# Kernel tuning notes

Hardware: AMD Instinct MI355X
Metric: run time of the kernel (lower is better)

## Reference

```python
import jax, jax.numpy as jnp
import numpy as np

B = 4096        # batch
KD = 64         # koopman_dim
NC = 24         # complex eigenvalue pairs
NR = 16         # real eigenvalues (KD = 2*NC + NR)
DT = 0.01       # delta_t
LC = 2 * NC     # complex net latent/out dim
LR = NR         # real net latent/out dim


def setup_inputs() -> dict:
    key = jax.random.key(0)
    ks = jax.random.split(key, 9)
    def w(k, o, i):
        return jax.random.normal(k, (o, i), dtype=jnp.float32) / np.sqrt(i)
    return {
        "x": jax.random.normal(ks[0], (B, 1, KD), dtype=jnp.float32),
        "Wc1": w(ks[1], LC, KD), "bc1": jnp.zeros((LC,), jnp.float32),
        "Wc2": w(ks[2], LC, LC), "bc2": jnp.zeros((LC,), jnp.float32),
        "Wr1": w(ks[3], LR, KD), "br1": jnp.zeros((LR,), jnp.float32),
        "Wr2": w(ks[4], LR, LR), "br2": jnp.zeros((LR,), jnp.float32),
        "T": 256,
    }


def reference(x, Wc1, bc1, Wc2, bc2, Wr1, br1, Wr2, br2, T):
    # Sequential Koopman rollout. Instead of materializing the [B,KD,KD]
    # block-diagonal K each step, apply the 2x2 rotation*decay blocks and the
    # real decay directly (identical math, no dense matmul).
    dt = jnp.float32(DT)

    def step(y, _):
        # complex parametrization MLP: [B,KD] -> [B,2*NC]
        co = jnp.tanh(y @ Wc1.T + bc1) @ Wc2.T + bc2
        co = co.reshape(-1, NC, 2)
        mu, omega = co[..., 0], co[..., 1]          # [B,NC] each
        scale = jnp.exp(dt * mu)
        c = jnp.cos(dt * omega) * scale             # cos*exp
        s = jnp.sin(dt * omega) * scale             # sin*exp
        yc = y[:, :2 * NC].reshape(-1, NC, 2)       # paired complex coords
        new_c = jnp.stack(
            [c * yc[..., 0] - s * yc[..., 1],
             s * yc[..., 0] + c * yc[..., 1]], axis=-1
        ).reshape(-1, 2 * NC)
        # real parametrization MLP: [B,KD] -> [B,NR]
        re = jnp.tanh(y @ Wr1.T + br1) @ Wr2.T + br2
        new_r = jnp.exp(dt * re) * y[:, 2 * NC:]
        y_new = jnp.concatenate([new_c, new_r], axis=-1)
        return y_new, y_new

    y0 = x[:, 0, :]
    _, Ys = jax.lax.scan(step, y0, None, length=T)  # [T,B,KD]
    return jnp.swapaxes(Ys, 0, 1)                   # [B,T,KD]
```

## Files before the change

kernel.cpp:

```cpp
#include <hip/hip_runtime.h>

#define NB    4096
#define TSTEP 256
#define EPB   8
#define DTC   0.01f

typedef _Float16 h8 __attribute__((ext_vector_type(8)));
typedef _Float16 h4 __attribute__((ext_vector_type(4)));
typedef float    f4 __attribute__((ext_vector_type(4)));

__device__ __forceinline__ float fast_tanh(float a) {
    float t = fminf(a * 2.885390082f, 126.0f);
    float E = __builtin_amdgcn_exp2f(t);
    return (E - 1.0f) * __builtin_amdgcn_rcpf(E + 1.0f);
}
__device__ __forceinline__ float texp(float m) {
    return fmaf(m, fmaf(m, fmaf(m, 1.0f/6.0f, 0.5f), 1.0f), 1.0f);
}

__device__ __forceinline__ void lds_barrier() {
    asm volatile("s_waitcnt lgkmcnt(0)" ::: "memory");
    __builtin_amdgcn_s_barrier();
    asm volatile("" ::: "memory");
}

#define U16B  2304

__global__ void __launch_bounds__(256)
koopman_kernel(const float* __restrict__ x,
               const float* __restrict__ Wc1, const float* __restrict__ bc1,
               const float* __restrict__ Wc2, const float* __restrict__ bc2,
               const float* __restrict__ Wr1, const float* __restrict__ br1,
               const float* __restrict__ Wr2, const float* __restrict__ br2,
               float* __restrict__ out)
{
    const int tid  = threadIdx.x;
    const int lane = tid & 63;
    const int w    = tid >> 6;
    const int blk  = blockIdx.x;

    __shared__ __align__(16) unsigned char L[U16B * 2];

    const int e  = lane & 15;
    const int es = e & (EPB - 1);
    const int g  = lane >> 4;

    const int fa = 16*w + e;
    h8 a1lo, a1hi, a2lo, a2hi;
    {
        const float* r1 = (fa < 48) ? (Wc1 + fa*64) : (Wr1 + (fa-48)*64);
        #pragma unroll
        for (int i = 0; i < 8; ++i) {
            a1lo[i] = (_Float16)r1[8*g + i];
            a1hi[i] = (_Float16)r1[32 + 8*g + i];
        }
        #pragma unroll
        for (int i = 0; i < 8; ++i) {
            const int k0 = 8*g + i, k1 = k0 + 32;
            float v0, v1;
            if (fa < 48) {
                v0 = (k0 < 48) ? Wc2[fa*48 + k0] : 0.0f;
                v1 = (k1 < 48) ? Wc2[fa*48 + k1] : 0.0f;
            } else {
                v0 = (k0 >= 48) ? Wr2[(fa-48)*16 + (k0-48)] : 0.0f;
                v1 = (k1 >= 48) ? Wr2[(fa-48)*16 + (k1-48)] : 0.0f;
            }
            a2lo[i] = (_Float16)v0;
            a2hi[i] = (_Float16)v1;
        }
    }
    float b1v[4], b2v[4], ys[4];
    #pragma unroll
    for (int r = 0; r < 4; ++r) {
        const int f = 16*w + 4*g + r;
        b1v[r] = (f < 48) ? bc1[f] : br1[f-48];
        b2v[r] = (f < 48) ? bc2[f] : br2[f-48];
        ys[r]  = x[(blk*EPB + es)*64 + f];
    }
    const bool cwave = (w < 3);

    const int rdoff = e*144 + 16*g;
    const int wroff = e*144 + (16*w + 4*g)*2;
    float* gp = out + (size_t)(blk*EPB + es) * (TSTEP*64) + 16*w + 4*g;
    const bool do_store = (e < EPB);

    {
        const int row = tid >> 4, col4 = (tid & 15) * 4;
        const f4 xv = *reinterpret_cast<const f4*>(x + (blk*EPB + (row & (EPB-1)))*64 + col4);
        h4 p; p[0]=(_Float16)xv[0]; p[1]=(_Float16)xv[1]; p[2]=(_Float16)xv[2]; p[3]=(_Float16)xv[3];
        *reinterpret_cast<h4*>(L + row*144 + col4*2) = p;
    }
    __syncthreads();

    for (int t = 0; t < TSTEP; ++t) {
        const h8 by0 = *reinterpret_cast<const h8*>(L + rdoff);
        const h8 by1 = *reinterpret_cast<const h8*>(L + rdoff + 64);
        f4 aL = {b1v[0], b1v[1], b1v[2], b1v[3]};
        f4 aH = {0.0f, 0.0f, 0.0f, 0.0f};
        aL = __builtin_amdgcn_mfma_f32_16x16x32_f16(a1lo, by0, aL, 0, 0, 0);
        aH = __builtin_amdgcn_mfma_f32_16x16x32_f16(a1hi, by1, aH, 0, 0, 0);
        const f4 a = aL + aH;
        h4 up;
        up[0]=(_Float16)fast_tanh(a[0]); up[1]=(_Float16)fast_tanh(a[1]);
        up[2]=(_Float16)fast_tanh(a[2]); up[3]=(_Float16)fast_tanh(a[3]);
        *reinterpret_cast<h4*>(L + U16B + wroff) = up;
        lds_barrier();

        const h8 bu0 = *reinterpret_cast<const h8*>(L + U16B + rdoff);
        const h8 bu1 = *reinterpret_cast<const h8*>(L + U16B + rdoff + 64);
        f4 cL = {b2v[0], b2v[1], b2v[2], b2v[3]};
        f4 cH = {0.0f, 0.0f, 0.0f, 0.0f};
        cL = __builtin_amdgcn_mfma_f32_16x16x32_f16(a2lo, bu0, cL, 0, 0, 0);
        cH = __builtin_amdgcn_mfma_f32_16x16x32_f16(a2hi, bu1, cH, 0, 0, 0);
        const f4 c = cL + cH;

        if (cwave) {
            const float m0 = DTC * c[0], x0 = DTC * c[1];
            const float m1 = DTC * c[2], x1 = DTC * c[3];
            const float E0 = texp(m0), E1 = texp(m1);
            const float q0 = x0*x0, q1 = x1*x1;
            float sp0 = fmaf(q0, 1.0f/120.0f, -1.0f/6.0f); sp0 = fmaf(q0, sp0, 1.0f);
            float cp0 = fmaf(q0, 1.0f/24.0f,  -0.5f);      cp0 = fmaf(q0, cp0, 1.0f);
            float sp1 = fmaf(q1, 1.0f/120.0f, -1.0f/6.0f); sp1 = fmaf(q1, sp1, 1.0f);
            float cp1 = fmaf(q1, 1.0f/24.0f,  -0.5f);      cp1 = fmaf(q1, cp1, 1.0f);
            const float s0 = E0 * x0 * sp0, c0v = E0 * cp0;
            const float s1 = E1 * x1 * sp1, c1v = E1 * cp1;
            const float n0 = c0v*ys[0] - s0*ys[1];
            const float n1 = s0*ys[0] + c0v*ys[1];
            const float n2 = c1v*ys[2] - s1*ys[3];
            const float n3 = s1*ys[2] + c1v*ys[3];
            ys[0]=n0; ys[1]=n1; ys[2]=n2; ys[3]=n3;
        } else {
            ys[0] *= texp(DTC * c[0]);
            ys[1] *= texp(DTC * c[1]);
            ys[2] *= texp(DTC * c[2]);
            ys[3] *= texp(DTC * c[3]);
        }

        h4 yp;
        yp[0]=(_Float16)ys[0]; yp[1]=(_Float16)ys[1]; yp[2]=(_Float16)ys[2]; yp[3]=(_Float16)ys[3];
        *reinterpret_cast<h4*>(L + wroff) = yp;
        if (do_store) {
            f4 yv = {ys[0], ys[1], ys[2], ys[3]};
            *reinterpret_cast<f4*>(gp) = yv;
        }
        gp += 64;
        lds_barrier();
    }
}

extern "C" void kernel_launch(void* const* d_in, const int* in_sizes, int n_in,
                              void* d_out, int out_size, void* d_ws, size_t ws_size,
                              hipStream_t stream) {
    const float* x   = (const float*)d_in[0];
    const float* Wc1 = (const float*)d_in[1];
    const float* bc1 = (const float*)d_in[2];
    const float* Wc2 = (const float*)d_in[3];
    const float* bc2 = (const float*)d_in[4];
    const float* Wr1 = (const float*)d_in[5];
    const float* br1 = (const float*)d_in[6];
    const float* Wr2 = (const float*)d_in[7];
    const float* br2 = (const float*)d_in[8];
    float* out = (float*)d_out;

    koopman_kernel<<<dim3(NB / EPB), dim3(256), 0, stream>>>(
        x, Wc1, bc1, Wc2, bc2, Wr1, br1, Wr2, br2, out);
}
```

Measured before the change: 143.4 us.

## Compute full hidden layer per wave to drop mid-step barrier, double-buffer state

Each wave now computes all 64 hidden units of the first layer redundantly with four MFMA pairs, then feeds the tanh outputs directly as register operands to the second MFMA. This removes the LDS round-trip and the barrier between the two layers. The state buffer in LDS is double-buffered so only one barrier per step remains. Blocks now process 16 batch elements instead of 8 (halving grid size and removing duplicated lanes), and waves_per_eu is pinned to 1. The cost is fourfold redundant first-layer MFMA work per wave and fewer blocks in flight.

```diff
diff --git a/kernel.cpp b/kernel.cpp
--- a/kernel.cpp
+++ b/kernel.cpp
@@ -2,7 +2,6 @@
 
 #define NB    4096
 #define TSTEP 256
-#define EPB   8
 #define DTC   0.01f
 
 typedef _Float16 h8 __attribute__((ext_vector_type(8)));
@@ -17,16 +16,17 @@
 __device__ __forceinline__ float texp(float m) {
     return fmaf(m, fmaf(m, fmaf(m, 1.0f/6.0f, 0.5f), 1.0f), 1.0f);
 }
-
+__device__ __forceinline__ float W2v(const float* Wc2, const float* Wr2, int C, int U) {
+    if (C < 48) return (U < 48) ? Wc2[C*48 + U] : 0.0f;
+    return (U >= 48) ? Wr2[(C-48)*16 + (U-48)] : 0.0f;
+}
 __device__ __forceinline__ void lds_barrier() {
     asm volatile("s_waitcnt lgkmcnt(0)" ::: "memory");
     __builtin_amdgcn_s_barrier();
     asm volatile("" ::: "memory");
 }
 
-#define U16B  2304
-
-__global__ void __launch_bounds__(256)
+__global__ void __launch_bounds__(256) __attribute__((amdgpu_waves_per_eu(1, 1)))
 koopman_kernel(const float* __restrict__ x,
                const float* __restrict__ Wc1, const float* __restrict__ bc1,
                const float* __restrict__ Wc2, const float* __restrict__ bc2,
@@ -37,114 +37,119 @@
     const int tid  = threadIdx.x;
     const int lane = tid & 63;
     const int w    = tid >> 6;
+    const int e    = lane & 15;
+    const int g    = lane >> 4;
     const int blk  = blockIdx.x;
 
-    __shared__ __align__(16) unsigned char L[U16B * 2];
+    __shared__ __align__(16) _Float16 Y[2][16 * 72];
 
-    const int e  = lane & 15;
-    const int es = e & (EPB - 1);
-    const int g  = lane >> 4;
-
-    const int fa = 16*w + e;
-    h8 a1lo, a1hi, a2lo, a2hi;
+    h8 a1[4][2];
+    #pragma unroll
+    for (int q = 0; q < 4; ++q) {
+        const int F = 16*q + e;
+        const float* row1 = (F < 48) ? (Wc1 + F*64) : (Wr1 + (F-48)*64);
+        #pragma unroll
+        for (int h = 0; h < 2; ++h)
+            #pragma unroll
+            for (int i = 0; i < 8; ++i)
+                a1[q][h][i] = (_Float16)row1[32*h + 8*g + i];
+    }
+    h8 a2[2];
     {
-        const float* r1 = (fa < 48) ? (Wc1 + fa*64) : (Wr1 + (fa-48)*64);
+        const int C = 16*w + e;
         #pragma unroll
-        for (int i = 0; i < 8; ++i) {
-            a1lo[i] = (_Float16)r1[8*g + i];
-            a1hi[i] = (_Float16)r1[32 + 8*g + i];
+        for (int h = 0; h < 2; ++h)
+            #pragma unroll
+            for (int i = 0; i < 8; ++i) {
+                const int U = 16*(2*h + (i >> 2)) + 4*g + (i & 3);
+                a2[h][i] = (_Float16)W2v(Wc2, Wr2, C, U);
+            }
+    }
+    f4 b1f[4], b2f;
+    #pragma unroll
+    for (int q = 0; q < 4; ++q)
+        #pragma unroll
+        for (int r = 0; r < 4; ++r) {
+            const int F = 16*q + 4*g + r;
+            b1f[q][r] = (F < 48) ? bc1[F] : br1[F-48];
         }
-        #pragma unroll
-        for (int i = 0; i < 8; ++i) {
-            const int k0 = 8*g + i, k1 = k0 + 32;
-            float v0, v1;
-            if (fa < 48) {
-                v0 = (k0 < 48) ? Wc2[fa*48 + k0] : 0.0f;
-                v1 = (k1 < 48) ? Wc2[fa*48 + k1] : 0.0f;
-            } else {
-                v0 = (k0 >= 48) ? Wr2[(fa-48)*16 + (k0-48)] : 0.0f;
-                v1 = (k1 >= 48) ? Wr2[(fa-48)*16 + (k1-48)] : 0.0f;
-            }
-            a2lo[i] = (_Float16)v0;
-            a2hi[i] = (_Float16)v1;
-        }
-    }
-    float b1v[4], b2v[4], ys[4];
     #pragma unroll
     for (int r = 0; r < 4; ++r) {
-        const int f = 16*w + 4*g + r;
-        b1v[r] = (f < 48) ? bc1[f] : br1[f-48];
-        b2v[r] = (f < 48) ? bc2[f] : br2[f-48];
-        ys[r]  = x[(blk*EPB + es)*64 + f];
+        const int C = 16*w + 4*g + r;
+        b2f[r] = (C < 48) ? bc2[C] : br2[C-48];
     }
-    const bool cwave = (w < 3);
 
-    const int rdoff = e*144 + 16*g;
-    const int wroff = e*144 + (16*w + 4*g)*2;
-    float* gp = out + (size_t)(blk*EPB + es) * (TSTEP*64) + 16*w + 4*g;
-    const bool do_store = (e < EPB);
+    float ys[4];
+    #pragma unroll
+    for (int r = 0; r < 4; ++r)
+        ys[r] = x[(size_t)(blk*16 + e)*64 + 16*w + 4*g + r];
 
     {
         const int row = tid >> 4, col4 = (tid & 15) * 4;
-        const f4 xv = *reinterpret_cast<const f4*>(x + (blk*EPB + (row & (EPB-1)))*64 + col4);
+        const f4 xv = *reinterpret_cast<const f4*>(x + (size_t)(blk*16 + row)*64 + col4);
         h4 p; p[0]=(_Float16)xv[0]; p[1]=(_Float16)xv[1]; p[2]=(_Float16)xv[2]; p[3]=(_Float16)xv[3];
-        *reinterpret_cast<h4*>(L + row*144 + col4*2) = p;
+        *reinterpret_cast<h4*>(&Y[0][row*72 + col4]) = p;
     }
     __syncthreads();
 
+    const bool cwave = (w < 3);
+    float* gps = out + (size_t)(blk*16 + e) * (TSTEP*64) + 16*w + 4*g;
+
     for (int t = 0; t < TSTEP; ++t) {
-        const h8 by0 = *reinterpret_cast<const h8*>(L + rdoff);
-        const h8 by1 = *reinterpret_cast<const h8*>(L + rdoff + 64);
-        f4 aL = {b1v[0], b1v[1], b1v[2], b1v[3]};
-        f4 aH = {0.0f, 0.0f, 0.0f, 0.0f};
-        aL = __builtin_amdgcn_mfma_f32_16x16x32_f16(a1lo, by0, aL, 0, 0, 0);
-        aH = __builtin_amdgcn_mfma_f32_16x16x32_f16(a1hi, by1, aH, 0, 0, 0);
-        const f4 a = aL + aH;
-        h4 up;
-        up[0]=(_Float16)fast_tanh(a[0]); up[1]=(_Float16)fast_tanh(a[1]);
-        up[2]=(_Float16)fast_tanh(a[2]); up[3]=(_Float16)fast_tanh(a[3]);
-        *reinterpret_cast<h4*>(L + U16B + wroff) = up;
-        lds_barrier();
+        const _Float16* yb = &Y[t & 1][e * 72];
+        const h8 by0 = *reinterpret_cast<const h8*>(yb + 8*g);
+        const h8 by1 = *reinterpret_cast<const h8*>(yb + 32 + 8*g);
 
-        const h8 bu0 = *reinterpret_cast<const h8*>(L + U16B + rdoff);
-        const h8 bu1 = *reinterpret_cast<const h8*>(L + U16B + rdoff + 64);
-        f4 cL = {b2v[0], b2v[1], b2v[2], b2v[3]};
-        f4 cH = {0.0f, 0.0f, 0.0f, 0.0f};
-        cL = __builtin_amdgcn_mfma_f32_16x16x32_f16(a2lo, bu0, cL, 0, 0, 0);
-        cH = __builtin_amdgcn_mfma_f32_16x16x32_f16(a2hi, bu1, cH, 0, 0, 0);
-        const f4 c = cL + cH;
+        f4 acc1[4];
+        #pragma unroll
+        for (int q = 0; q < 4; ++q)
+            acc1[q] = __builtin_amdgcn_mfma_f32_16x16x32_f16(a1[q][0], by0, b1f[q], 0, 0, 0);
+        #pragma unroll
+        for (int q = 0; q < 4; ++q)
+            acc1[q] = __builtin_amdgcn_mfma_f32_16x16x32_f16(a1[q][1], by1, acc1[q], 0, 0, 0);
+
+        h8 bu0, bu1;
+        #pragma unroll
+        for (int i = 0; i < 8; ++i) bu0[i] = (_Float16)fast_tanh(acc1[(i >> 2)    ][i & 3]);
+        #pragma unroll
+        for (int i = 0; i < 8; ++i) bu1[i] = (_Float16)fast_tanh(acc1[2 + (i >> 2)][i & 3]);
+
+        f4 acc2 = __builtin_amdgcn_mfma_f32_16x16x32_f16(a2[0], bu0, b2f, 0, 0, 0);
+        acc2    = __builtin_amdgcn_mfma_f32_16x16x32_f16(a2[1], bu1, acc2, 0, 0, 0);
 
         if (cwave) {
-            const float m0 = DTC * c[0], x0 = DTC * c[1];
-            const float m1 = DTC * c[2], x1 = DTC * c[3];
-            const float E0 = texp(m0), E1 = texp(m1);
+            const float E0 = texp(DTC * acc2[0]);
+            const float x0 = DTC * acc2[1];
+            const float E1 = texp(DTC * acc2[2]);
+            const float x1 = DTC * acc2[3];
             const float q0 = x0*x0, q1 = x1*x1;
             float sp0 = fmaf(q0, 1.0f/120.0f, -1.0f/6.0f); sp0 = fmaf(q0, sp0, 1.0f);
             float cp0 = fmaf(q0, 1.0f/24.0f,  -0.5f);      cp0 = fmaf(q0, cp0, 1.0f);
             float sp1 = fmaf(q1, 1.0f/120.0f, -1.0f/6.0f); sp1 = fmaf(q1, sp1, 1.0f);
             float cp1 = fmaf(q1, 1.0f/24.0f,  -0.5f);      cp1 = fmaf(q1, cp1, 1.0f);
-            const float s0 = E0 * x0 * sp0, c0v = E0 * cp0;
-            const float s1 = E1 * x1 * sp1, c1v = E1 * cp1;
-            const float n0 = c0v*ys[0] - s0*ys[1];
-            const float n1 = s0*ys[0] + c0v*ys[1];
-            const float n2 = c1v*ys[2] - s1*ys[3];
-            const float n3 = s1*ys[2] + c1v*ys[3];
+            const float s0 = E0 * x0 * sp0, c0 = E0 * cp0;
+            const float s1 = E1 * x1 * sp1, c1 = E1 * cp1;
+            const float n0 = fmaf(c0, ys[0], -s0 * ys[1]);
+            const float n1 = fmaf(s0, ys[0],  c0 * ys[1]);
+            const float n2 = fmaf(c1, ys[2], -s1 * ys[3]);
+            const float n3 = fmaf(s1, ys[2],  c1 * ys[3]);
             ys[0]=n0; ys[1]=n1; ys[2]=n2; ys[3]=n3;
         } else {
-            ys[0] *= texp(DTC * c[0]);
-            ys[1] *= texp(DTC * c[1]);
-            ys[2] *= texp(DTC * c[2]);
-            ys[3] *= texp(DTC * c[3]);
+            ys[0] *= texp(DTC * acc2[0]);
+            ys[1] *= texp(DTC * acc2[1]);
+            ys[2] *= texp(DTC * acc2[2]);
+            ys[3] *= texp(DTC * acc2[3]);
         }
 
         h4 yp;
-        yp[0]=(_Float16)ys[0]; yp[1]=(_Float16)ys[1]; yp[2]=(_Float16)ys[2]; yp[3]=(_Float16)ys[3];
-        *reinterpret_cast<h4*>(L + wroff) = yp;
-        if (do_store) {
-            f4 yv = {ys[0], ys[1], ys[2], ys[3]};
-            *reinterpret_cast<f4*>(gp) = yv;
-        }
-        gp += 64;
+        yp[0]=(_Float16)ys[0]; yp[1]=(_Float16)ys[1];
+        yp[2]=(_Float16)ys[2]; yp[3]=(_Float16)ys[3];
+        *reinterpret_cast<h4*>(&Y[(t + 1) & 1][e*72 + 16*w + 4*g]) = yp;
+
+        const f4 sv = {ys[0], ys[1], ys[2], ys[3]};
+        *reinterpret_cast<f4*>(gps) = sv;
+        gps += 64;
+
         lds_barrier();
     }
 }
@@ -163,6 +168,6 @@
     const float* br2 = (const float*)d_in[8];
     float* out = (float*)d_out;
 
-    koopman_kernel<<<dim3(NB / EPB), dim3(256), 0, stream>>>(
+    koopman_kernel<<<dim3(NB / 16), dim3(256), 0, stream>>>(
         x, Wc1, bc1, Wc2, bc2, Wr1, br1, Wr2, br2, out);
 }
```

Result: slower. 154.9 us (+8.0%).
